# Optimization experiments

Hardware: AMD Instinct MI355X
Metric: run time of the kernel (lower is better)

Reference implementation:

```python
import jax, jax.numpy as jnp
import numpy as np

B, S, E, H, NQ, FF = 2, 2048, 768, 12, 8, 3072
DK = E // H
EPS = 1e-5


def _layernorm(x, g, b):
    m = jnp.mean(x, axis=-1, keepdims=True)
    v = jnp.mean((x - m) ** 2, axis=-1, keepdims=True)
    return (x - m) * jax.lax.rsqrt(v + EPS) * g + b


def setup_inputs() -> dict:
    key = jax.random.key(0)
    ks = jax.random.split(key, 12)
    s = 0.02
    return {
        'x': jax.random.normal(ks[0], (B, S, E), dtype=jnp.float32),
        'W_o': jax.random.normal(ks[1], (E, E), dtype=jnp.float32) * s,
        'b_o': jnp.zeros((E,), dtype=jnp.float32),
        'g1': jnp.ones((E,), dtype=jnp.float32),
        'be1': jnp.zeros((E,), dtype=jnp.float32),
        'g2': jnp.ones((E,), dtype=jnp.float32),
        'be2': jnp.zeros((E,), dtype=jnp.float32),
        'ry': jax.random.normal(ks[2], (NQ,), dtype=jnp.float32),
        'W1': jax.random.normal(ks[3], (NQ, FF), dtype=jnp.float32) * s,
        'b1': jnp.zeros((FF,), dtype=jnp.float32),
        'W2': jax.random.normal(ks[4], (FF, E), dtype=jnp.float32) * s,
        'b2': jnp.zeros((E,), dtype=jnp.float32),
    }


def reference(x, W_o, b_o, g1, be1, g2, be2, ry, W1, b1, W2, b2):
    # --- multi-head self-attention (q = k = v = x, no QKV projection) ---
    q = x.reshape(B, S, H, DK).transpose(0, 2, 1, 3)  # [B,H,S,DK]
    scores = jnp.einsum('bhqd,bhkd->bhqk', q, q) / jnp.sqrt(jnp.float32(DK))
    attn = jax.nn.softmax(scores, axis=-1)
    out = jnp.einsum('bhqk,bhkd->bhqd', attn, q)
    out = out.transpose(0, 2, 1, 3).reshape(B, S, E)
    attn_out = out @ W_o + b_o

    x = _layernorm(x + attn_out, g1, be1)

    # --- quantum FFN: per-wire RX(x_i) encode, RY(ry_i), <Z> = cos(x_i)*cos(ry_i) ---
    q_meas = jnp.cos(x[..., :NQ]) * jnp.cos(ry)  # [B,S,NQ]
    ffn_out = jax.nn.relu(q_meas @ W1 + b1) @ W2 + b2

    return _layernorm(x + ffn_out, g2, be2)
```

## Files before the change

kernel.cpp:

```cpp
#include <hip/hip_runtime.h>
#include <hip/hip_bf16.h>

#define B_  2
#define S_  2048
#define E_  768
#define H_  12
#define DK_ 64
#define NQ_ 8
#define FF_ 3072
#define EPS_ 1e-5f

typedef __attribute__((ext_vector_type(8))) short short8;
typedef __attribute__((ext_vector_type(4))) short shortv4;
typedef __attribute__((ext_vector_type(4))) float f32x4;
typedef __hip_bfloat16 bf16;

__device__ __forceinline__ bf16 f2bh(float f) { return __float2bfloat16(f); }
__device__ __forceinline__ short f2b(float f) {
    bf16 h = __float2bfloat16(f);
    return *reinterpret_cast<short*>(&h);
}
__device__ __forceinline__ float b2f(short s) {
    bf16 h = *reinterpret_cast<bf16*>(&s);
    return __bfloat162float(h);
}

__device__ __forceinline__ int swz(int row, int col) {
    return (col & 7) | ((((col >> 3) ^ (row & 7)) & 7) << 3);
}

__device__ __forceinline__ f32x4 mfma16(short8 a, short8 b, f32x4 c) {
    return __builtin_amdgcn_mfma_f32_16x16x32_bf16(a, b, c, 0, 0, 0);
}

__device__ __forceinline__ void gload16(const bf16* g, bf16* l) {
    __builtin_amdgcn_global_load_lds(
        (__attribute__((address_space(1))) void*)g,
        (__attribute__((address_space(3))) void*)l, 16, 0, 0);
}

__global__ __launch_bounds__(256) void prep_xall(const float* __restrict__ x,
                                                 bf16* __restrict__ xb,
                                                 bf16* __restrict__ xT) {
    __shared__ float tile[32][33];
    int e0 = blockIdx.x * 32, s0 = blockIdx.y * 32;
    int tx = threadIdx.x & 31, ty = threadIdx.x >> 5;
    int b = s0 >> 11, sl0 = s0 & 2047;
#pragma unroll
    for (int i = 0; i < 4; i++) {
        int row = ty + i * 8;
        float v = x[(size_t)(s0 + row) * E_ + e0 + tx];
        tile[row][tx] = v;
        xb[(size_t)(s0 + row) * E_ + e0 + tx] = f2bh(v);
    }
    __syncthreads();
#pragma unroll
    for (int i = 0; i < 4; i++) {
        int row = ty + i * 8;
        xT[((size_t)b * E_ + e0 + row) * S_ + sl0 + tx] = f2bh(tile[tx][row]);
    }
}

__global__ __launch_bounds__(256) void prep_cvt(const float* __restrict__ x,
                                                bf16* __restrict__ xb, int n4) {
    int i = blockIdx.x * 256 + threadIdx.x;
    if (i >= n4) return;
    float4 f = *(const float4*)(x + (size_t)i * 4);
    short4 sv;
    sv.x = f2b(f.x); sv.y = f2b(f.y); sv.z = f2b(f.z); sv.w = f2b(f.w);
    *(short4*)((short*)xb + (size_t)i * 4) = sv;
}

__global__ __launch_bounds__(256) void transpose_cvt(const float* __restrict__ W,
                                                     bf16* __restrict__ WT,
                                                     int K, int N) {
    __shared__ float tile[32][33];
    int k0 = blockIdx.y * 32, n0 = blockIdx.x * 32;
    int tx = threadIdx.x & 31, ty = threadIdx.x >> 5;
#pragma unroll
    for (int i = 0; i < 4; i++) {
        int row = ty + i * 8;
        tile[row][tx] = W[(size_t)(k0 + row) * N + n0 + tx];
    }
    __syncthreads();
#pragma unroll
    for (int i = 0; i < 4; i++) {
        int row = ty + i * 8;
        WT[(size_t)(n0 + row) * K + k0 + tx] = f2bh(tile[tx][row]);
    }
}

__global__ __launch_bounds__(256) void prep_w1t(const float* __restrict__ W1,
                                                bf16* __restrict__ W1bT) {
    int k = blockIdx.x * 256 + threadIdx.x;
    if (k >= FF_) return;
    short8 v;
#pragma unroll
    for (int i = 0; i < NQ_; i++) v[i] = f2b(W1[(size_t)i * FF_ + k]);
    *(short8*)(W1bT + (size_t)k * NQ_) = v;
}

template<bool XT>
__global__ __launch_bounds__(256) void attn_kernel(const bf16* __restrict__ xb,
                                                   const bf16* __restrict__ xT,
                                                   bf16* __restrict__ out) {
    const int qtiles = S_ / 64;
    const int nwg = B_ * H_ * qtiles;
    const int NT = S_ / 64;
    int o = blockIdx.x;
    int blk = (o & 7) * (nwg >> 3) + (o >> 3);
    int qt = blk % qtiles;
    int hh = (blk / qtiles) % H_;
    int bb = blk / (qtiles * H_);
    const bf16* base = xb + (size_t)bb * S_ * E_ + hh * DK_;
    const bf16* baseT = xT + ((size_t)bb * E_ + hh * DK_) * S_;

    __shared__ __align__(16) bf16 Ks[2][64][64];
    __shared__ __align__(16) bf16 Vt[2][64][64];
    __shared__ __align__(16) bf16 Pl[4][16][68];

    int t = threadIdx.x;
    int w = t >> 6, l = t & 63, c = l & 15, g = l >> 4;

    short8 qf[2];
    {
        const bf16* qp = base + (size_t)(qt * 64 + w * 16 + c) * E_;
#pragma unroll
        for (int kh = 0; kh < 2; kh++) {
            short8 v = *(const short8*)(qp + kh * 32 + g * 8);
#pragma unroll
            for (int j = 0; j < 8; j++) v[j] = f2b(b2f(v[j]) * 0.18033688f);
            qf[kh] = v;
        }
    }

    f32x4 oacc[4];
    float lsum = 0.f;
#pragma unroll
    for (int n = 0; n < 4; n++) oacc[n] = (f32x4){0.f, 0.f, 0.f, 0.f};

    int rr = l >> 3;
    int scol = ((l & 7) ^ (rr & 7)) * 8;
    const bf16* srcK = base + (size_t)(w * 16 + rr) * E_ + scol;
    const bf16* srcV = baseT + (size_t)(w * 16 + rr) * S_ + scol;

    int skey = t & 63, scb0 = t >> 6;
    short8 preK[2];

    if (XT) {
        gload16(srcK, &Ks[0][w * 16][0]);
        gload16(srcK + 8 * E_, &Ks[0][w * 16 + 8][0]);
        gload16(srcV, &Vt[0][w * 16][0]);
        gload16(srcV + 8 * S_, &Vt[0][w * 16 + 8][0]);
    } else {
#pragma unroll
        for (int it = 0; it < 2; it++)
            preK[it] = *(const short8*)(base + (size_t)skey * E_ + (scb0 + it * 4) * 8);
#pragma unroll
        for (int it = 0; it < 2; it++) {
            int cb = scb0 + it * 4;
            *(short8*)&Ks[0][skey][swz(skey, cb * 8)] = preK[it];
#pragma unroll
            for (int j = 0; j < 8; j++) {
                int d = cb * 8 + j;
                short sv = preK[it][j];
                Vt[0][d][swz(d, skey)] = *reinterpret_cast<bf16*>(&sv);
            }
        }
#pragma unroll
        for (int it = 0; it < 2; it++)
            preK[it] = *(const short8*)(base + (size_t)(64 + skey) * E_ + (scb0 + it * 4) * 8);
    }
    __syncthreads();

    int cur = 0;
    for (int kt = 0; kt < NT; kt++, cur ^= 1) {
        int nxt = cur ^ 1;
        if (kt + 1 < NT) {
            if (XT) {
                const bf16* sK = srcK + (size_t)(kt + 1) * 64 * E_;
                const bf16* sV = srcV + (kt + 1) * 64;
                gload16(sK, &Ks[nxt][w * 16][0]);
                gload16(sK + 8 * E_, &Ks[nxt][w * 16 + 8][0]);
                gload16(sV, &Vt[nxt][w * 16][0]);
                gload16(sV + 8 * S_, &Vt[nxt][w * 16 + 8][0]);
            } else {
#pragma unroll
                for (int it = 0; it < 2; it++) {
                    int cb = scb0 + it * 4;
                    *(short8*)&Ks[nxt][skey][swz(skey, cb * 8)] = preK[it];
#pragma unroll
                    for (int j = 0; j < 8; j++) {
                        int d = cb * 8 + j;
                        short sv = preK[it][j];
                        Vt[nxt][d][swz(d, skey)] = *reinterpret_cast<bf16*>(&sv);
                    }
                }
            }
        }
        if (!XT && kt + 2 < NT) {
#pragma unroll
            for (int it = 0; it < 2; it++)
                preK[it] = *(const short8*)(base + (size_t)((kt + 2) * 64 + skey) * E_ + (scb0 + it * 4) * 8);
        }

        f32x4 sfr[4];
        __builtin_amdgcn_s_setprio(1);
#pragma unroll
        for (int n = 0; n < 4; n++) {
            sfr[n] = (f32x4){0.f, 0.f, 0.f, 0.f};
#pragma unroll
            for (int kh = 0; kh < 2; kh++) {
                const short8 bfr = *(const short8*)&Ks[cur][n * 16 + c][swz(n * 16 + c, kh * 32 + g * 8)];
                sfr[n] = mfma16(bfr, qf[kh], sfr[n]);
            }
        }
        __builtin_amdgcn_s_setprio(0);

#pragma unroll
        for (int n = 0; n < 4; n++) {
            float pv[4];
#pragma unroll
            for (int jj = 0; jj < 4; jj++) pv[jj] = exp2f(sfr[n][jj]);
            lsum += (pv[0] + pv[1]) + (pv[2] + pv[3]);
            shortv4 pk;
#pragma unroll
            for (int jj = 0; jj < 4; jj++) pk[jj] = f2b(pv[jj]);
            *(shortv4*)&Pl[w][c][swz(c, n * 16 + g * 4)] = pk;
        }

        __builtin_amdgcn_s_setprio(1);
#pragma unroll
        for (int ks = 0; ks < 2; ks++) {
            short8 vb[4];
#pragma unroll
            for (int dn = 0; dn < 4; dn++)
                vb[dn] = *(const short8*)&Vt[cur][dn * 16 + c][swz(dn * 16 + c, ks * 32 + g * 8)];
            const short8 pa = *(const short8*)&Pl[w][c][swz(c, ks * 32 + g * 8)];
#pragma unroll
            for (int dn = 0; dn < 4; dn++)
                oacc[dn] = mfma16(pa, vb[dn], oacc[dn]);
        }
        __builtin_amdgcn_s_setprio(0);
        __syncthreads();
    }

#pragma unroll
    for (int msk = 16; msk < 64; msk <<= 1) lsum += __shfl_xor(lsum, msk);
#pragma unroll
    for (int jj = 0; jj < 4; jj++) {
        float inv = 1.f / __shfl(lsum, g * 4 + jj);
        size_t ro = ((size_t)bb * S_ + qt * 64 + w * 16 + g * 4 + jj) * E_ + hh * DK_;
#pragma unroll
        for (int dn = 0; dn < 4; dn++)
            out[ro + dn * 16 + c] = f2bh(oacc[dn][jj] * inv);
    }
}

__global__ __launch_bounds__(256) void gemm_bf16(const bf16* __restrict__ A,
                                                 const bf16* __restrict__ BT,
                                                 const float* __restrict__ bias,
                                                 bf16* __restrict__ C,
                                                 int M, int N, int K) {
    __shared__ __align__(16) bf16 As2[2][64][64];
    __shared__ __align__(16) bf16 Bs2[2][64][64];
    int nbx = gridDim.x, nwg = nbx * gridDim.y;
    int id = blockIdx.y * nbx + blockIdx.x;
    int id2 = (nwg & 7) ? id : ((id & 7) * (nwg >> 3) + (id >> 3));
    int row0 = (id2 / nbx) * 64, col0 = (id2 % nbx) * 64;
    int t = threadIdx.x, w = t >> 6, l = t & 63, c = l & 15, g = l >> 4;

    f32x4 acc[4];
#pragma unroll
    for (int n = 0; n < 4; n++) acc[n] = (f32x4){0.f, 0.f, 0.f, 0.f};

    int srow = w * 16 + (l >> 3);
    int scol = ((l & 7) ^ ((l >> 3) & 7)) * 8;
    const bf16* apR0 = A + (size_t)(row0 + srow) * K + scol;
    const bf16* apR1 = A + (size_t)(row0 + srow + 8) * K + scol;
    const bf16* bpR0 = BT + (size_t)(col0 + srow) * K + scol;
    const bf16* bpR1 = BT + (size_t)(col0 + srow + 8) * K + scol;

    gload16(apR0, &As2[0][w * 16][0]);
    gload16(apR1, &As2[0][w * 16 + 8][0]);
    gload16(bpR0, &Bs2[0][w * 16][0]);
    gload16(bpR1, &Bs2[0][w * 16 + 8][0]);
    __syncthreads();

    int cur = 0;
    for (int k0 = 0; k0 < K; k0 += 64, cur ^= 1) {
        int nxt = cur ^ 1;
        if (k0 + 64 < K) {
            gload16(apR0 + k0 + 64, &As2[nxt][w * 16][0]);
            gload16(apR1 + k0 + 64, &As2[nxt][w * 16 + 8][0]);
            gload16(bpR0 + k0 + 64, &Bs2[nxt][w * 16][0]);
            gload16(bpR1 + k0 + 64, &Bs2[nxt][w * 16 + 8][0]);
        }
#pragma unroll
        for (int kh = 0; kh < 2; kh++) {
            const short8 af = *(const short8*)&As2[cur][w * 16 + c][swz(w * 16 + c, kh * 32 + g * 8)];
#pragma unroll
            for (int n = 0; n < 4; n++) {
                const short8 bfr = *(const short8*)&Bs2[cur][n * 16 + c][swz(n * 16 + c, kh * 32 + g * 8)];
                acc[n] = mfma16(af, bfr, acc[n]);
            }
        }
        __syncthreads();
    }
#pragma unroll
    for (int jj = 0; jj < 4; jj++) {
        int row = row0 + w * 16 + g * 4 + jj;
#pragma unroll
        for (int n = 0; n < 4; n++) {
            int col = col0 + n * 16 + c;
            C[(size_t)row * N + col] = f2bh(acc[n][jj] + bias[col]);
        }
    }
}

__global__ __launch_bounds__(256) void gemm2_mfma(const float* __restrict__ xln,
                                                  const float* __restrict__ ry,
                                                  const bf16* __restrict__ W1bT,
                                                  const float* __restrict__ b1,
                                                  const bf16* __restrict__ W2bT,
                                                  const float* __restrict__ b2,
                                                  bf16* __restrict__ C) {
    __shared__ __align__(16) bf16 As[64][68];
    __shared__ __align__(16) bf16 Bs[2][64][64];
    __shared__ __align__(16) bf16 W1t[2][64][8];
    __shared__ __align__(16) bf16 qm_s[64][8];
    const int nbx = E_ / 64;
    const int nwg = nbx * (B_ * S_ / 64);
    int id = blockIdx.y * nbx + blockIdx.x;
    int id2 = (id & 7) * (nwg >> 3) + (id >> 3);
    int row0 = (id2 / nbx) * 64, col0 = (id2 % nbx) * 64;
    int t = threadIdx.x, w = t >> 6, l = t & 63, c = l & 15, g = l >> 4;

    if (t < 64) {
        const float* xp = xln + (size_t)(row0 + t) * E_;
#pragma unroll
        for (int i = 0; i < NQ_; i++)
            qm_s[t][i] = f2bh(cosf(xp[i]) * cosf(ry[i]));
    }

    f32x4 acc[4];
#pragma unroll
    for (int n = 0; n < 4; n++) acc[n] = (f32x4){0.f, 0.f, 0.f, 0.f};

    int srow = w * 16 + (l >> 3);
    int scol = ((l & 7) ^ ((l >> 3) & 7)) * 8;
    const bf16* bpR0 = W2bT + (size_t)(col0 + srow) * FF_ + scol;
    const bf16* bpR1 = W2bT + (size_t)(col0 + srow + 8) * FF_ + scol;

    gload16(bpR0, &Bs[0][w * 16][0]);
    gload16(bpR1, &Bs[0][w * 16 + 8][0]);
    short8 preW;
    if (t < 64) {
        preW = *(const short8*)(W1bT + (size_t)t * NQ_);
        *(short8*)&W1t[0][t][0] = preW;
        preW = *(const short8*)(W1bT + (size_t)(64 + t) * NQ_);
    }
    __syncthreads();

    short8 zz = {0, 0, 0, 0, 0, 0, 0, 0};
    short8 aq = zz;
    if (g == 0) aq = *(const short8*)&qm_s[w * 16 + c][0];

    int cur = 0;
    for (int k0 = 0; k0 < FF_; k0 += 64, cur ^= 1) {
        f32x4 b1v[4];
#pragma unroll
        for (int n = 0; n < 4; n++)
            b1v[n] = *(const f32x4*)(b1 + k0 + n * 16 + g * 4);

        int nxt = cur ^ 1;
        if (k0 + 64 < FF_) {
            gload16(bpR0 + k0 + 64, &Bs[nxt][w * 16][0]);
            gload16(bpR1 + k0 + 64, &Bs[nxt][w * 16 + 8][0]);
            if (t < 64) *(short8*)&W1t[nxt][t][0] = preW;
        }
        if (k0 + 128 < FF_) {
            if (t < 64) preW = *(const short8*)(W1bT + (size_t)(k0 + 128 + t) * NQ_);
        }

        f32x4 zero4 = {0.f, 0.f, 0.f, 0.f};
        int r = w * 16 + c;
#pragma unroll
        for (int n = 0; n < 4; n++) {
            short8 bw = zz;
            if (g == 0) bw = *(const short8*)&W1t[cur][n * 16 + c][0];
            f32x4 hfr = mfma16(bw, aq, zero4);
            shortv4 pk;
#pragma unroll
            for (int jj = 0; jj < 4; jj++)
                pk[jj] = f2b(fmaxf(hfr[jj] + b1v[n][jj], 0.f));
            *(shortv4*)&As[r][swz(r, n * 16 + g * 4)] = pk;
        }

#pragma unroll
        for (int kh = 0; kh < 2; kh++) {
            const short8 af = *(const short8*)&As[w * 16 + c][swz(w * 16 + c, kh * 32 + g * 8)];
#pragma unroll
            for (int n = 0; n < 4; n++) {
                const short8 bfr = *(const short8*)&Bs[cur][n * 16 + c][swz(n * 16 + c, kh * 32 + g * 8)];
                acc[n] = mfma16(af, bfr, acc[n]);
            }
        }
        __syncthreads();
    }
#pragma unroll
    for (int jj = 0; jj < 4; jj++) {
        int row = row0 + w * 16 + g * 4 + jj;
#pragma unroll
        for (int n = 0; n < 4; n++) {
            int col = col0 + n * 16 + c;
            C[(size_t)row * E_ + col] = f2bh(acc[n][jj] + b2[col]);
        }
    }
}

__global__ __launch_bounds__(256) void gemm2_fused(const float* __restrict__ xln,
                                                   const float* __restrict__ ry,
                                                   const float* __restrict__ W1,
                                                   const float* __restrict__ b1,
                                                   const float* __restrict__ W2,
                                                   const float* __restrict__ b2,
                                                   bf16* __restrict__ C) {
    __shared__ __align__(16) bf16 As[64][64];
    __shared__ __align__(16) bf16 Bst[64][64];
    __shared__ float qmS[64][NQ_];
    int row0 = blockIdx.y * 64, col0 = blockIdx.x * 64;
    int t = threadIdx.x, w = t >> 6, l = t & 63, c = l & 15, g = l >> 4;

    for (int idx = t; idx < 64 * NQ_; idx += 256) {
        int r = idx >> 3, i = idx & 7;
        qmS[r][i] = cosf(xln[(size_t)(row0 + r) * E_ + i]) * cosf(ry[i]);
    }

    f32x4 acc[4];
#pragma unroll
    for (int n = 0; n < 4; n++) acc[n] = (f32x4){0.f, 0.f, 0.f, 0.f};

    int kl = t & 63, rg = (t >> 6) * 16;
    int brow = t >> 4, bcol = (t & 15) * 4;

    for (int k0 = 0; k0 < FF_; k0 += 64) {
        __syncthreads();
        {
            float w1v[NQ_];
#pragma unroll
            for (int i = 0; i < NQ_; i++) w1v[i] = W1[i * FF_ + k0 + kl];
            float b1v = b1[k0 + kl];
#pragma unroll
            for (int r16 = 0; r16 < 16; r16++) {
                int r = rg + r16;
                float sh = b1v;
#pragma unroll
                for (int i = 0; i < NQ_; i++) sh += qmS[r][i] * w1v[i];
                As[r][swz(r, kl)] = f2bh(fmaxf(sh, 0.f));
            }
        }
#pragma unroll
        for (int it = 0; it < 4; it++) {
            int kk = brow + it * 16;
            float4 v = *(const float4*)(W2 + (size_t)(k0 + kk) * E_ + col0 + bcol);
            Bst[bcol + 0][swz(bcol + 0, kk)] = f2bh(v.x);
            Bst[bcol + 1][swz(bcol + 1, kk)] = f2bh(v.y);
            Bst[bcol + 2][swz(bcol + 2, kk)] = f2bh(v.z);
            Bst[bcol + 3][swz(bcol + 3, kk)] = f2bh(v.w);
        }
        __syncthreads();
#pragma unroll
        for (int kh = 0; kh < 2; kh++) {
            const short8 af = *(const short8*)&As[w * 16 + c][swz(w * 16 + c, kh * 32 + g * 8)];
#pragma unroll
            for (int n = 0; n < 4; n++) {
                const short8 bfr = *(const short8*)&Bst[n * 16 + c][swz(n * 16 + c, kh * 32 + g * 8)];
                acc[n] = mfma16(af, bfr, acc[n]);
            }
        }
    }
#pragma unroll
    for (int jj = 0; jj < 4; jj++) {
        int row = row0 + w * 16 + g * 4 + jj;
#pragma unroll
        for (int n = 0; n < 4; n++) {
            int col = col0 + n * 16 + c;
            C[(size_t)row * E_ + col] = f2bh(acc[n][jj] + b2[col]);
        }
    }
}

__global__ __launch_bounds__(256) void ln_add_b(const float* __restrict__ X,
                                                const bf16* __restrict__ Yb,
                                                const float* __restrict__ g,
                                                const float* __restrict__ be,
                                                float* __restrict__ out) {
    int r = blockIdx.x;
    const size_t off = (size_t)r * E_;
    int t = threadIdx.x;
    float v[3];
    float s = 0.f, s2 = 0.f;
#pragma unroll
    for (int j = 0; j < 3; j++) {
        int e = t + j * 256;
        float val = X[off + e] + __bfloat162float(Yb[off + e]);
        v[j] = val; s += val; s2 += val * val;
    }
#pragma unroll
    for (int msk = 32; msk > 0; msk >>= 1) {
        s += __shfl_xor(s, msk);
        s2 += __shfl_xor(s2, msk);
    }
    __shared__ float red[8];
    int lane = t & 63, wv = t >> 6;
    if (lane == 0) { red[wv] = s; red[4 + wv] = s2; }
    __syncthreads();
    if (t == 0) {
        red[0] = red[0] + red[1] + red[2] + red[3];
        red[4] = red[4] + red[5] + red[6] + red[7];
    }
    __syncthreads();
    float mean = red[0] * (1.f / E_);
    float var = red[4] * (1.f / E_) - mean * mean;
    float inv = rsqrtf(var + EPS_);
#pragma unroll
    for (int j = 0; j < 3; j++) {
        int e = t + j * 256;
        out[off + e] = (v[j] - mean) * inv * g[e] + be[e];
    }
}

extern "C" void kernel_launch(void* const* d_in, const int* in_sizes, int n_in,
                              void* d_out, int out_size, void* d_ws, size_t ws_size,
                              hipStream_t stream) {
    const float* x   = (const float*)d_in[0];
    const float* W_o = (const float*)d_in[1];
    const float* b_o = (const float*)d_in[2];
    const float* g1  = (const float*)d_in[3];
    const float* be1 = (const float*)d_in[4];
    const float* g2  = (const float*)d_in[5];
    const float* be2 = (const float*)d_in[6];
    const float* ry  = (const float*)d_in[7];
    const float* W1  = (const float*)d_in[8];
    const float* b1  = (const float*)d_in[9];
    const float* W2  = (const float*)d_in[10];
    const float* b2  = (const float*)d_in[11];
    float* out = (float*)d_out;

    const size_t BSE = (size_t)B_ * S_ * E_;
    char* ws = (char*)d_ws;

    const size_t FAST_NEED = 43696128;
    bool fast = ws_size >= FAST_NEED;

    bf16* xb    = (bf16*)(ws + 0);
    bf16* attnb = (bf16*)(ws + 6291456);
    bf16* WobT  = fast ? (bf16*)(ws + 12582912) : (bf16*)(ws + 18874368);
    bf16* W2bT  = (bf16*)(ws + 13762560);
    bf16* tmp1b = fast ? (bf16*)(ws + 18481152) : (bf16*)(ws + 12582912);
    float* xln  = (float*)(ws + (fast ? 24772608 : 20054016));
    bf16* W1bT  = (bf16*)(ws + 37355520);
    bf16* xT    = (bf16*)(ws + 37404672);
    bf16* tmp2b = tmp1b;

    if (fast) {
        prep_xall<<<dim3(E_ / 32, B_ * S_ / 32), 256, 0, stream>>>(x, xb, xT);
        transpose_cvt<<<dim3(E_ / 32, FF_ / 32), 256, 0, stream>>>(W2, W2bT, FF_, E_);
        prep_w1t<<<dim3(FF_ / 256), 256, 0, stream>>>(W1, W1bT);
    } else {
        prep_cvt<<<dim3((int)((BSE / 4 + 255) / 256)), 256, 0, stream>>>(x, xb, (int)(BSE / 4));
    }
    transpose_cvt<<<dim3(E_ / 32, E_ / 32), 256, 0, stream>>>(W_o, WobT, E_, E_);

    if (fast)
        attn_kernel<true><<<dim3(B_ * H_ * (S_ / 64)), 256, 0, stream>>>(xb, xT, attnb);
    else
        attn_kernel<false><<<dim3(B_ * H_ * (S_ / 64)), 256, 0, stream>>>(xb, xb, attnb);

    gemm_bf16<<<dim3(E_ / 64, (B_ * S_) / 64), 256, 0, stream>>>(
        attnb, WobT, b_o, tmp1b, B_ * S_, E_, E_);
    ln_add_b<<<dim3(B_ * S_), 256, 0, stream>>>(x, tmp1b, g1, be1, xln);

    if (fast) {
        gemm2_mfma<<<dim3(E_ / 64, (B_ * S_) / 64), 256, 0, stream>>>(
            xln, ry, W1bT, b1, W2bT, b2, tmp2b);
    } else {
        gemm2_fused<<<dim3(E_ / 64, (B_ * S_) / 64), 256, 0, stream>>>(
            xln, ry, W1, b1, W2, b2, tmp2b);
    }
    ln_add_b<<<dim3(B_ * S_), 256, 0, stream>>>(xln, tmp2b, g2, be2, out);
}
```

Baseline: 149.4 us.

## Split FFN GEMM K dimension in two and sum partials in LayerNorm

Doubles the gemm2 grid so each workgroup reduces over half of the FF dimension. The two bf16 partial results go to separate workspace buffers, and a new LayerNorm kernel adds both into the residual. This raises the number of concurrent workgroups and shortens each one's serial K loop. In exchange it adds extra partial-output memory traffic and a second bf16 rounding of intermediate sums.

```diff
diff --git a/kernel.cpp b/kernel.cpp
--- a/kernel.cpp
+++ b/kernel.cpp
@@ -324,16 +324,21 @@
                                                   const float* __restrict__ b1,
                                                   const bf16* __restrict__ W2bT,
                                                   const float* __restrict__ b2,
-                                                  bf16* __restrict__ C) {
+                                                  bf16* __restrict__ Cp0,
+                                                  bf16* __restrict__ Cp1) {
     __shared__ __align__(16) bf16 As[64][68];
     __shared__ __align__(16) bf16 Bs[2][64][64];
     __shared__ __align__(16) bf16 W1t[2][64][8];
     __shared__ __align__(16) bf16 qm_s[64][8];
     const int nbx = E_ / 64;
-    const int nwg = nbx * (B_ * S_ / 64);
+    const int nwg = nbx * (B_ * S_ / 64) * 2;
+    const int KS = FF_ / 2;
     int id = blockIdx.y * nbx + blockIdx.x;
     int id2 = (id & 7) * (nwg >> 3) + (id >> 3);
-    int row0 = (id2 / nbx) * 64, col0 = (id2 % nbx) * 64;
+    int col0 = (id2 % nbx) * 64;
+    int rp = id2 / nbx;
+    int row0 = (rp >> 1) * 64;
+    int kb = (rp & 1) * KS;
     int t = threadIdx.x, w = t >> 6, l = t & 63, c = l & 15, g = l >> 4;
 
     if (t < 64) {
@@ -349,16 +354,16 @@
 
     int srow = w * 16 + (l >> 3);
     int scol = ((l & 7) ^ ((l >> 3) & 7)) * 8;
-    const bf16* bpR0 = W2bT + (size_t)(col0 + srow) * FF_ + scol;
-    const bf16* bpR1 = W2bT + (size_t)(col0 + srow + 8) * FF_ + scol;
+    const bf16* bpR0 = W2bT + (size_t)(col0 + srow) * FF_ + kb + scol;
+    const bf16* bpR1 = W2bT + (size_t)(col0 + srow + 8) * FF_ + kb + scol;
 
     gload16(bpR0, &Bs[0][w * 16][0]);
     gload16(bpR1, &Bs[0][w * 16 + 8][0]);
     short8 preW;
     if (t < 64) {
-        preW = *(const short8*)(W1bT + (size_t)t * NQ_);
+        preW = *(const short8*)(W1bT + (size_t)(kb + t) * NQ_);
         *(short8*)&W1t[0][t][0] = preW;
-        preW = *(const short8*)(W1bT + (size_t)(64 + t) * NQ_);
+        preW = *(const short8*)(W1bT + (size_t)(kb + 64 + t) * NQ_);
     }
     __syncthreads();
 
@@ -367,20 +372,20 @@
     if (g == 0) aq = *(const short8*)&qm_s[w * 16 + c][0];
 
     int cur = 0;
-    for (int k0 = 0; k0 < FF_; k0 += 64, cur ^= 1) {
+    for (int k0 = 0; k0 < KS; k0 += 64, cur ^= 1) {
         f32x4 b1v[4];
 #pragma unroll
         for (int n = 0; n < 4; n++)
-            b1v[n] = *(const f32x4*)(b1 + k0 + n * 16 + g * 4);
+            b1v[n] = *(const f32x4*)(b1 + kb + k0 + n * 16 + g * 4);
 
         int nxt = cur ^ 1;
-        if (k0 + 64 < FF_) {
+        if (k0 + 64 < KS) {
             gload16(bpR0 + k0 + 64, &Bs[nxt][w * 16][0]);
             gload16(bpR1 + k0 + 64, &Bs[nxt][w * 16 + 8][0]);
             if (t < 64) *(short8*)&W1t[nxt][t][0] = preW;
         }
-        if (k0 + 128 < FF_) {
-            if (t < 64) preW = *(const short8*)(W1bT + (size_t)(k0 + 128 + t) * NQ_);
+        if (k0 + 128 < KS) {
+            if (t < 64) preW = *(const short8*)(W1bT + (size_t)(kb + k0 + 128 + t) * NQ_);
         }
 
         f32x4 zero4 = {0.f, 0.f, 0.f, 0.f};
@@ -408,13 +413,16 @@
         }
         __syncthreads();
     }
+    bf16* Cp = (rp & 1) ? Cp1 : Cp0;
+    bool addb = (rp & 1) == 0;
 #pragma unroll
     for (int jj = 0; jj < 4; jj++) {
         int row = row0 + w * 16 + g * 4 + jj;
 #pragma unroll
         for (int n = 0; n < 4; n++) {
             int col = col0 + n * 16 + c;
-            C[(size_t)row * E_ + col] = f2bh(acc[n][jj] + b2[col]);
+            float v = acc[n][jj] + (addb ? b2[col] : 0.f);
+            Cp[(size_t)row * E_ + col] = f2bh(v);
         }
     }
 }
@@ -505,6 +513,48 @@
     for (int j = 0; j < 3; j++) {
         int e = t + j * 256;
         float val = X[off + e] + __bfloat162float(Yb[off + e]);
+        v[j] = val; s += val; s2 += val * val;
+    }
+#pragma unroll
+    for (int msk = 32; msk > 0; msk >>= 1) {
+        s += __shfl_xor(s, msk);
+        s2 += __shfl_xor(s2, msk);
+    }
+    __shared__ float red[8];
+    int lane = t & 63, wv = t >> 6;
+    if (lane == 0) { red[wv] = s; red[4 + wv] = s2; }
+    __syncthreads();
+    if (t == 0) {
+        red[0] = red[0] + red[1] + red[2] + red[3];
+        red[4] = red[4] + red[5] + red[6] + red[7];
+    }
+    __syncthreads();
+    float mean = red[0] * (1.f / E_);
+    float var = red[4] * (1.f / E_) - mean * mean;
+    float inv = rsqrtf(var + EPS_);
+#pragma unroll
+    for (int j = 0; j < 3; j++) {
+        int e = t + j * 256;
+        out[off + e] = (v[j] - mean) * inv * g[e] + be[e];
+    }
+}
+
+__global__ __launch_bounds__(256) void ln_add2_b(const float* __restrict__ X,
+                                                 const bf16* __restrict__ Y0,
+                                                 const bf16* __restrict__ Y1,
+                                                 const float* __restrict__ g,
+                                                 const float* __restrict__ be,
+                                                 float* __restrict__ out) {
+    int r = blockIdx.x;
+    const size_t off = (size_t)r * E_;
+    int t = threadIdx.x;
+    float v[3];
+    float s = 0.f, s2 = 0.f;
+#pragma unroll
+    for (int j = 0; j < 3; j++) {
+        int e = t + j * 256;
+        float val = X[off + e] + __bfloat162float(Y0[off + e])
+                               + __bfloat162float(Y1[off + e]);
         v[j] = val; s += val; s2 += val * val;
     }
 #pragma unroll
@@ -562,6 +612,8 @@
     float* xln  = (float*)(ws + (fast ? 24772608 : 20054016));
     bf16* W1bT  = (bf16*)(ws + 37355520);
     bf16* xT    = (bf16*)(ws + 37404672);
+    bf16* Cp0   = (bf16*)(ws + 0);
+    bf16* Cp1   = (bf16*)(ws + 6291456);
     bf16* tmp2b = tmp1b;
 
     if (fast) {
@@ -583,11 +635,12 @@
     ln_add_b<<<dim3(B_ * S_), 256, 0, stream>>>(x, tmp1b, g1, be1, xln);
 
     if (fast) {
-        gemm2_mfma<<<dim3(E_ / 64, (B_ * S_) / 64), 256, 0, stream>>>(
-            xln, ry, W1bT, b1, W2bT, b2, tmp2b);
+        gemm2_mfma<<<dim3(E_ / 64, (B_ * S_) / 64 * 2), 256, 0, stream>>>(
+            xln, ry, W1bT, b1, W2bT, b2, Cp0, Cp1);
+        ln_add2_b<<<dim3(B_ * S_), 256, 0, stream>>>(xln, Cp0, Cp1, g2, be2, out);
     } else {
         gemm2_fused<<<dim3(E_ / 64, (B_ * S_) / 64), 256, 0, stream>>>(
             xln, ry, W1, b1, W2, b2, tmp2b);
-    }
-    ln_add_b<<<dim3(B_ * S_), 256, 0, stream>>>(xln, tmp2b, g2, be2, out);
-}
+        ln_add_b<<<dim3(B_ * S_), 256, 0, stream>>>(xln, tmp2b, g2, be2, out);
+    }
+}
```

New measurement: 159.2 us. 6.6% more time.

## Split attention over two key halves and add a combine kernel

Applied to the files above, without the earlier changes.

Replaces the single attention kernel with a split-K variant. Each key half is handled by its own workgroup, which doubles the grid. Each half writes an unnormalized bf16 partial output plus per-row softmax sums, and a new combine kernel adds the halves and normalizes. The split kernel uses one LDS buffer with load-after-sync instead of double-buffered prefetch, so load and compute may overlap less. It also adds an extra kernel launch, extra global round trips, and bf16 rounding of unnormalized partial results.

```diff
diff --git a/kernel.cpp b/kernel.cpp
--- a/kernel.cpp
+++ b/kernel.cpp
@@ -100,10 +100,156 @@
     *(short8*)(W1bT + (size_t)k * NQ_) = v;
 }
 
-template<bool XT>
-__global__ __launch_bounds__(256) void attn_kernel(const bf16* __restrict__ xb,
-                                                   const bf16* __restrict__ xT,
-                                                   bf16* __restrict__ out) {
+__global__ __launch_bounds__(256) void attn_split(const bf16* __restrict__ xb,
+                                                  const bf16* __restrict__ xT,
+                                                  bf16* __restrict__ Op0,
+                                                  bf16* __restrict__ Op1,
+                                                  float* __restrict__ lbuf) {
+    const int qtiles = S_ / 64;
+    const int nwg = B_ * H_ * qtiles * 2;
+    const int NT = S_ / 128;
+    int o = blockIdx.x;
+    int blk = (o & 7) * (nwg >> 3) + (o >> 3);
+    int qt = blk % qtiles;
+    int hh = (blk / qtiles) % H_;
+    int bb = (blk / (qtiles * H_)) % B_;
+    int ksl = blk / (qtiles * H_ * B_);
+    int kb = ksl * (S_ / 2);
+    const bf16* base = xb + (size_t)bb * S_ * E_ + hh * DK_;
+    const bf16* baseT = xT + ((size_t)bb * E_ + hh * DK_) * S_;
+
+    __shared__ __align__(16) bf16 Ks[64][64];
+    __shared__ __align__(16) bf16 Vt[64][64];
+    __shared__ __align__(16) bf16 Pl[4][16][64];
+
+    int t = threadIdx.x;
+    int w = t >> 6, l = t & 63, c = l & 15, g = l >> 4;
+
+    short8 qf[2];
+    {
+        const bf16* qp = base + (size_t)(qt * 64 + w * 16 + c) * E_;
+#pragma unroll
+        for (int kh = 0; kh < 2; kh++) {
+            short8 v = *(const short8*)(qp + kh * 32 + g * 8);
+#pragma unroll
+            for (int j = 0; j < 8; j++) v[j] = f2b(b2f(v[j]) * 0.18033688f);
+            qf[kh] = v;
+        }
+    }
+
+    f32x4 oacc[4];
+    float lsum = 0.f;
+#pragma unroll
+    for (int n = 0; n < 4; n++) oacc[n] = (f32x4){0.f, 0.f, 0.f, 0.f};
+
+    int rr = l >> 3;
+    int scol = ((l & 7) ^ (rr & 7)) * 8;
+    const bf16* srcK = base + (size_t)(kb + w * 16 + rr) * E_ + scol;
+    const bf16* srcV = baseT + (size_t)(w * 16 + rr) * S_ + kb + scol;
+
+    gload16(srcK, &Ks[w * 16][0]);
+    gload16(srcK + 8 * E_, &Ks[w * 16 + 8][0]);
+    gload16(srcV, &Vt[w * 16][0]);
+    gload16(srcV + 8 * S_, &Vt[w * 16 + 8][0]);
+    __syncthreads();
+
+    for (int kt = 0; kt < NT; kt++) {
+        f32x4 sfr[4];
+        __builtin_amdgcn_s_setprio(1);
+#pragma unroll
+        for (int n = 0; n < 4; n++) {
+            sfr[n] = (f32x4){0.f, 0.f, 0.f, 0.f};
+#pragma unroll
+            for (int kh = 0; kh < 2; kh++) {
+                const short8 bfr = *(const short8*)&Ks[n * 16 + c][swz(n * 16 + c, kh * 32 + g * 8)];
+                sfr[n] = mfma16(bfr, qf[kh], sfr[n]);
+            }
+        }
+        __builtin_amdgcn_s_setprio(0);
+
+#pragma unroll
+        for (int n = 0; n < 4; n++) {
+            float pv[4];
+#pragma unroll
+            for (int jj = 0; jj < 4; jj++) pv[jj] = exp2f(sfr[n][jj]);
+            lsum += (pv[0] + pv[1]) + (pv[2] + pv[3]);
+            shortv4 pk;
+#pragma unroll
+            for (int jj = 0; jj < 4; jj++) pk[jj] = f2b(pv[jj]);
+            *(shortv4*)&Pl[w][c][swz(c, n * 16 + g * 4)] = pk;
+        }
+
+        __builtin_amdgcn_s_setprio(1);
+#pragma unroll
+        for (int ks = 0; ks < 2; ks++) {
+            short8 vb[4];
+#pragma unroll
+            for (int dn = 0; dn < 4; dn++)
+                vb[dn] = *(const short8*)&Vt[dn * 16 + c][swz(dn * 16 + c, ks * 32 + g * 8)];
+            const short8 pa = *(const short8*)&Pl[w][c][swz(c, ks * 32 + g * 8)];
+#pragma unroll
+            for (int dn = 0; dn < 4; dn++)
+                oacc[dn] = mfma16(pa, vb[dn], oacc[dn]);
+        }
+        __builtin_amdgcn_s_setprio(0);
+        __syncthreads();
+
+        if (kt + 1 < NT) {
+            const bf16* sK = srcK + (size_t)(kt + 1) * 64 * E_;
+            const bf16* sV = srcV + (kt + 1) * 64;
+            gload16(sK, &Ks[w * 16][0]);
+            gload16(sK + 8 * E_, &Ks[w * 16 + 8][0]);
+            gload16(sV, &Vt[w * 16][0]);
+            gload16(sV + 8 * S_, &Vt[w * 16 + 8][0]);
+        }
+        __syncthreads();
+    }
+
+#pragma unroll
+    for (int msk = 16; msk < 64; msk <<= 1) lsum += __shfl_xor(lsum, msk);
+    if (g == 0)
+        lbuf[((size_t)(ksl * B_ + bb) * S_ + qt * 64 + w * 16 + c) * H_ + hh] = lsum;
+
+    bf16* outp = ksl ? Op1 : Op0;
+#pragma unroll
+    for (int jj = 0; jj < 4; jj++) {
+        size_t ro = ((size_t)bb * S_ + qt * 64 + w * 16 + g * 4 + jj) * E_ + hh * DK_;
+#pragma unroll
+        for (int dn = 0; dn < 4; dn++)
+            outp[ro + dn * 16 + c] = f2bh(oacc[dn][jj]);
+    }
+}
+
+__global__ __launch_bounds__(256) void attn_combine(const bf16* __restrict__ Op0,
+                                                    const bf16* __restrict__ Op1,
+                                                    const float* __restrict__ lbuf,
+                                                    bf16* __restrict__ attnb) {
+    int r0 = blockIdx.x * 4;
+    int t = threadIdx.x;
+#pragma unroll
+    for (int j = 0; j < 3; j++) {
+        int ci = t + j * 256;
+        int rr = r0 + ci / 192;
+        int e4 = (ci % 192) * 4;
+        int b = rr >> 11, s = rr & (S_ - 1);
+        int h = e4 >> 6;
+        float l0 = lbuf[((size_t)b * S_ + s) * H_ + h];
+        float l1 = lbuf[((size_t)(B_ + b) * S_ + s) * H_ + h];
+        float inv = 1.f / (l0 + l1);
+        size_t off = (size_t)rr * E_ + e4;
+        short4 a = *(const short4*)((const short*)Op0 + off);
+        short4 bq = *(const short4*)((const short*)Op1 + off);
+        short4 ov;
+        ov.x = f2b((b2f(a.x) + b2f(bq.x)) * inv);
+        ov.y = f2b((b2f(a.y) + b2f(bq.y)) * inv);
+        ov.z = f2b((b2f(a.z) + b2f(bq.z)) * inv);
+        ov.w = f2b((b2f(a.w) + b2f(bq.w)) * inv);
+        *(short4*)((short*)attnb + off) = ov;
+    }
+}
+
+__global__ __launch_bounds__(256) void attn_kernel_fb(const bf16* __restrict__ xb,
+                                                      bf16* __restrict__ out) {
     const int qtiles = S_ / 64;
     const int nwg = B_ * H_ * qtiles;
     const int NT = S_ / 64;
@@ -113,7 +259,6 @@
     int hh = (blk / qtiles) % H_;
     int bb = blk / (qtiles * H_);
     const bf16* base = xb + (size_t)bb * S_ * E_ + hh * DK_;
-    const bf16* baseT = xT + ((size_t)bb * E_ + hh * DK_) * S_;
 
     __shared__ __align__(16) bf16 Ks[2][64][64];
     __shared__ __align__(16) bf16 Vt[2][64][64];
@@ -139,73 +284,50 @@
 #pragma unroll
     for (int n = 0; n < 4; n++) oacc[n] = (f32x4){0.f, 0.f, 0.f, 0.f};
 
-    int rr = l >> 3;
-    int scol = ((l & 7) ^ (rr & 7)) * 8;
-    const bf16* srcK = base + (size_t)(w * 16 + rr) * E_ + scol;
-    const bf16* srcV = baseT + (size_t)(w * 16 + rr) * S_ + scol;
-
     int skey = t & 63, scb0 = t >> 6;
     short8 preK[2];
-
-    if (XT) {
-        gload16(srcK, &Ks[0][w * 16][0]);
-        gload16(srcK + 8 * E_, &Ks[0][w * 16 + 8][0]);
-        gload16(srcV, &Vt[0][w * 16][0]);
-        gload16(srcV + 8 * S_, &Vt[0][w * 16 + 8][0]);
-    } else {
-#pragma unroll
-        for (int it = 0; it < 2; it++)
-            preK[it] = *(const short8*)(base + (size_t)skey * E_ + (scb0 + it * 4) * 8);
-#pragma unroll
-        for (int it = 0; it < 2; it++) {
-            int cb = scb0 + it * 4;
-            *(short8*)&Ks[0][skey][swz(skey, cb * 8)] = preK[it];
-#pragma unroll
-            for (int j = 0; j < 8; j++) {
-                int d = cb * 8 + j;
-                short sv = preK[it][j];
-                Vt[0][d][swz(d, skey)] = *reinterpret_cast<bf16*>(&sv);
-            }
-        }
-#pragma unroll
-        for (int it = 0; it < 2; it++)
-            preK[it] = *(const short8*)(base + (size_t)(64 + skey) * E_ + (scb0 + it * 4) * 8);
-    }
+#pragma unroll
+    for (int it = 0; it < 2; it++)
+        preK[it] = *(const short8*)(base + (size_t)skey * E_ + (scb0 + it * 4) * 8);
+#pragma unroll
+    for (int it = 0; it < 2; it++) {
+        int cb = scb0 + it * 4;
+        *(short8*)&Ks[0][skey][swz(skey, cb * 8)] = preK[it];
+#pragma unroll
+        for (int j = 0; j < 8; j++) {
+            int d = cb * 8 + j;
+            short sv = preK[it][j];
+            Vt[0][d][swz(d, skey)] = *reinterpret_cast<bf16*>(&sv);
+        }
+    }
+#pragma unroll
+    for (int it = 0; it < 2; it++)
+        preK[it] = *(const short8*)(base + (size_t)(64 + skey) * E_ + (scb0 + it * 4) * 8);
     __syncthreads();
 
     int cur = 0;
     for (int kt = 0; kt < NT; kt++, cur ^= 1) {
         int nxt = cur ^ 1;
         if (kt + 1 < NT) {
-            if (XT) {
-                const bf16* sK = srcK + (size_t)(kt + 1) * 64 * E_;
-                const bf16* sV = srcV + (kt + 1) * 64;
-                gload16(sK, &Ks[nxt][w * 16][0]);
-                gload16(sK + 8 * E_, &Ks[nxt][w * 16 + 8][0]);
-                gload16(sV, &Vt[nxt][w * 16][0]);
-                gload16(sV + 8 * S_, &Vt[nxt][w * 16 + 8][0]);
-            } else {
-#pragma unroll
-                for (int it = 0; it < 2; it++) {
-                    int cb = scb0 + it * 4;
-                    *(short8*)&Ks[nxt][skey][swz(skey, cb * 8)] = preK[it];
-#pragma unroll
-                    for (int j = 0; j < 8; j++) {
-                        int d = cb * 8 + j;
-                        short sv = preK[it][j];
-                        Vt[nxt][d][swz(d, skey)] = *reinterpret_cast<bf16*>(&sv);
-                    }
+#pragma unroll
+            for (int it = 0; it < 2; it++) {
+                int cb = scb0 + it * 4;
+                *(short8*)&Ks[nxt][skey][swz(skey, cb * 8)] = preK[it];
+#pragma unroll
+                for (int j = 0; j < 8; j++) {
+                    int d = cb * 8 + j;
+                    short sv = preK[it][j];
+                    Vt[nxt][d][swz(d, skey)] = *reinterpret_cast<bf16*>(&sv);
                 }
             }
         }
-        if (!XT && kt + 2 < NT) {
+        if (kt + 2 < NT) {
 #pragma unroll
             for (int it = 0; it < 2; it++)
                 preK[it] = *(const short8*)(base + (size_t)((kt + 2) * 64 + skey) * E_ + (scb0 + it * 4) * 8);
         }
 
         f32x4 sfr[4];
-        __builtin_amdgcn_s_setprio(1);
 #pragma unroll
         for (int n = 0; n < 4; n++) {
             sfr[n] = (f32x4){0.f, 0.f, 0.f, 0.f};
@@ -215,8 +337,6 @@
                 sfr[n] = mfma16(bfr, qf[kh], sfr[n]);
             }
         }
-        __builtin_amdgcn_s_setprio(0);
-
 #pragma unroll
         for (int n = 0; n < 4; n++) {
             float pv[4];
@@ -228,8 +348,6 @@
             for (int jj = 0; jj < 4; jj++) pk[jj] = f2b(pv[jj]);
             *(shortv4*)&Pl[w][c][swz(c, n * 16 + g * 4)] = pk;
         }
-
-        __builtin_amdgcn_s_setprio(1);
 #pragma unroll
         for (int ks = 0; ks < 2; ks++) {
             short8 vb[4];
@@ -241,7 +359,6 @@
             for (int dn = 0; dn < 4; dn++)
                 oacc[dn] = mfma16(pa, vb[dn], oacc[dn]);
         }
-        __builtin_amdgcn_s_setprio(0);
         __syncthreads();
     }
 
@@ -558,10 +675,13 @@
     bf16* attnb = (bf16*)(ws + 6291456);
     bf16* WobT  = fast ? (bf16*)(ws + 12582912) : (bf16*)(ws + 18874368);
     bf16* W2bT  = (bf16*)(ws + 13762560);
-    bf16* tmp1b = fast ? (bf16*)(ws + 18481152) : (bf16*)(ws + 12582912);
-    float* xln  = (float*)(ws + (fast ? 24772608 : 20054016));
-    bf16* W1bT  = (bf16*)(ws + 37355520);
-    bf16* xT    = (bf16*)(ws + 37404672);
+    bf16* W1bT  = (bf16*)(ws + 18481152);
+    bf16* xT    = (bf16*)(ws + 18530304);
+    bf16* Op0   = (bf16*)(ws + 24821760);
+    bf16* Op1   = (bf16*)(ws + 31113216);
+    float* lbuf = (float*)(ws + 37404672);
+    bf16* tmp1b = fast ? (bf16*)(ws + 24821760) : (bf16*)(ws + 12582912);
+    float* xln  = (float*)(ws + (fast ? 31113216 : 20054016));
     bf16* tmp2b = tmp1b;
 
     if (fast) {
@@ -573,10 +693,13 @@
     }
     transpose_cvt<<<dim3(E_ / 32, E_ / 32), 256, 0, stream>>>(W_o, WobT, E_, E_);
 
-    if (fast)
-        attn_kernel<true><<<dim3(B_ * H_ * (S_ / 64)), 256, 0, stream>>>(xb, xT, attnb);
-    else
-        attn_kernel<false><<<dim3(B_ * H_ * (S_ / 64)), 256, 0, stream>>>(xb, xb, attnb);
+    if (fast) {
+        attn_split<<<dim3(B_ * H_ * (S_ / 64) * 2), 256, 0, stream>>>(
+            xb, xT, Op0, Op1, lbuf);
+        attn_combine<<<dim3(B_ * S_ / 4), 256, 0, stream>>>(Op0, Op1, lbuf, attnb);
+    } else {
+        attn_kernel_fb<<<dim3(B_ * H_ * (S_ / 64)), 256, 0, stream>>>(xb, attnb);
+    }
 
     gemm_bf16<<<dim3(E_ / 64, (B_ * S_) / 64), 256, 0, stream>>>(
         attnb, WobT, b_o, tmp1b, B_ * S_, E_, E_);
```

Result: slower. 154.5 us (+3.4%).

## Software-pipeline hidden-layer compute one K-step ahead of W2 MFMA in FFN kernel

Applied to the files above, without the earlier changes.

The fused FFN GEMM now computes the ReLU hidden tile for the next K-block (first-layer MFMA plus bias) while the current block's second-layer MFMAs run. It double-buffers the activation tile in shared memory and triple-buffers the W1 slices, with a prologue that fills the first tile. This is meant to hide the dependent hidden-tile latency behind the main MFMA chain, at the cost of more LDS and registers.

```diff
diff --git a/kernel.cpp b/kernel.cpp
--- a/kernel.cpp
+++ b/kernel.cpp
@@ -325,9 +325,9 @@
                                                   const bf16* __restrict__ W2bT,
                                                   const float* __restrict__ b2,
                                                   bf16* __restrict__ C) {
-    __shared__ __align__(16) bf16 As[64][68];
+    __shared__ __align__(16) bf16 As[2][64][68];
     __shared__ __align__(16) bf16 Bs[2][64][64];
-    __shared__ __align__(16) bf16 W1t[2][64][8];
+    __shared__ __align__(16) bf16 W1t[3][64][8];
     __shared__ __align__(16) bf16 qm_s[64][8];
     const int nbx = E_ / 64;
     const int nwg = nbx * (B_ * S_ / 64);
@@ -354,56 +354,83 @@
 
     gload16(bpR0, &Bs[0][w * 16][0]);
     gload16(bpR1, &Bs[0][w * 16 + 8][0]);
-    short8 preW;
     if (t < 64) {
-        preW = *(const short8*)(W1bT + (size_t)t * NQ_);
-        *(short8*)&W1t[0][t][0] = preW;
-        preW = *(const short8*)(W1bT + (size_t)(64 + t) * NQ_);
+        *(short8*)&W1t[0][t][0] = *(const short8*)(W1bT + (size_t)t * NQ_);
+        *(short8*)&W1t[1][t][0] = *(const short8*)(W1bT + (size_t)(64 + t) * NQ_);
     }
     __syncthreads();
 
-    short8 zz = {0, 0, 0, 0, 0, 0, 0, 0};
+    const short8 zz = {0, 0, 0, 0, 0, 0, 0, 0};
+    const f32x4 zero4 = {0.f, 0.f, 0.f, 0.f};
     short8 aq = zz;
     if (g == 0) aq = *(const short8*)&qm_s[w * 16 + c][0];
+    int r = w * 16 + c;
+
+    {
+        f32x4 b1v0[4];
+#pragma unroll
+        for (int n = 0; n < 4; n++)
+            b1v0[n] = *(const f32x4*)(b1 + n * 16 + g * 4);
+#pragma unroll
+        for (int n = 0; n < 4; n++) {
+            short8 bw = zz;
+            if (g == 0) bw = *(const short8*)&W1t[0][n * 16 + c][0];
+            f32x4 hfr = mfma16(bw, aq, zero4);
+            shortv4 pk;
+#pragma unroll
+            for (int jj = 0; jj < 4; jj++)
+                pk[jj] = f2b(fmaxf(hfr[jj] + b1v0[n][jj], 0.f));
+            *(shortv4*)&As[0][r][swz(r, n * 16 + g * 4)] = pk;
+        }
+    }
 
     int cur = 0;
     for (int k0 = 0; k0 < FF_; k0 += 64, cur ^= 1) {
-        f32x4 b1v[4];
-#pragma unroll
-        for (int n = 0; n < 4; n++)
-            b1v[n] = *(const f32x4*)(b1 + k0 + n * 16 + g * 4);
-
+        int kidx = k0 >> 6;
         int nxt = cur ^ 1;
+
         if (k0 + 64 < FF_) {
             gload16(bpR0 + k0 + 64, &Bs[nxt][w * 16][0]);
             gload16(bpR1 + k0 + 64, &Bs[nxt][w * 16 + 8][0]);
-            if (t < 64) *(short8*)&W1t[nxt][t][0] = preW;
-        }
-        if (k0 + 128 < FF_) {
-            if (t < 64) preW = *(const short8*)(W1bT + (size_t)(k0 + 128 + t) * NQ_);
-        }
-
-        f32x4 zero4 = {0.f, 0.f, 0.f, 0.f};
-        int r = w * 16 + c;
-#pragma unroll
-        for (int n = 0; n < 4; n++) {
-            short8 bw = zz;
-            if (g == 0) bw = *(const short8*)&W1t[cur][n * 16 + c][0];
-            f32x4 hfr = mfma16(bw, aq, zero4);
-            shortv4 pk;
-#pragma unroll
-            for (int jj = 0; jj < 4; jj++)
-                pk[jj] = f2b(fmaxf(hfr[jj] + b1v[n][jj], 0.f));
-            *(shortv4*)&As[r][swz(r, n * 16 + g * 4)] = pk;
+        }
+        if (k0 + 128 < FF_ && t < 64) {
+            *(short8*)&W1t[(kidx + 2) % 3][t][0] =
+                *(const short8*)(W1bT + (size_t)(k0 + 128 + t) * NQ_);
+        }
+
+        f32x4 hfr[4];
+        f32x4 b1v[4];
+        if (k0 + 64 < FF_) {
+            int sl = (kidx + 1) % 3;
+#pragma unroll
+            for (int n = 0; n < 4; n++)
+                b1v[n] = *(const f32x4*)(b1 + k0 + 64 + n * 16 + g * 4);
+#pragma unroll
+            for (int n = 0; n < 4; n++) {
+                short8 bw = zz;
+                if (g == 0) bw = *(const short8*)&W1t[sl][n * 16 + c][0];
+                hfr[n] = mfma16(bw, aq, zero4);
+            }
         }
 
 #pragma unroll
         for (int kh = 0; kh < 2; kh++) {
-            const short8 af = *(const short8*)&As[w * 16 + c][swz(w * 16 + c, kh * 32 + g * 8)];
+            const short8 af = *(const short8*)&As[cur][w * 16 + c][swz(w * 16 + c, kh * 32 + g * 8)];
 #pragma unroll
             for (int n = 0; n < 4; n++) {
                 const short8 bfr = *(const short8*)&Bs[cur][n * 16 + c][swz(n * 16 + c, kh * 32 + g * 8)];
                 acc[n] = mfma16(af, bfr, acc[n]);
+            }
+        }
+
+        if (k0 + 64 < FF_) {
+#pragma unroll
+            for (int n = 0; n < 4; n++) {
+                shortv4 pk;
+#pragma unroll
+                for (int jj = 0; jj < 4; jj++)
+                    pk[jj] = f2b(fmaxf(hfr[n][jj] + b1v[n][jj], 0.f));
+                *(shortv4*)&As[nxt][r][swz(r, n * 16 + g * 4)] = pk;
             }
         }
         __syncthreads();
```

Result: no change. 150.7 us (+0.8%).
